# Optimization experiments

Hardware: AMD Instinct MI355X
Metric: run time of the kernel (lower is better)

The kernel has to match this reference:

```python
import jax, jax.numpy as jnp
import numpy as np

DIM = 1024
HEADS = 16
DIM_HEAD = 64
INNER = HEADS * DIM_HEAD
VID_LEN = 10
IMG_H, IMG_W = 16, 16
KS, KT = 5, 7  # kernel_spatial, kernel_temporal (causal=True)
BATCH = 1
SEQ = VID_LEN * IMG_H * IMG_W + 1  # +1 from causal pad -> 2561


def nearby_mask_causal(T, H, W, ks, kt):
    # numpy replication of generate_nearby_mask(causal=True); static, setup-time only
    te = (kt - 1) // 2
    frame = H * W
    S = T * frame
    p = ks // 2
    tmpl = (np.arange(ks * ks) >= (ks * ks) // 2).reshape(ks, ks)
    m = np.ones((S, T, H + 2 * p, W + 2 * p), dtype=bool)
    for t in range(T):
        for h in range(H):
            for w in range(W):
                i = t * frame + h * W + w
                m[i, t, h:h + ks, w:w + ks] = tmpl
                m[i, max(0, t - te):t, h:h + ks, w:w + ks] = False
    m = m[:, :, p:-p, p:-p].reshape(S, S)
    m = np.roll(m, -1, axis=0)
    m = np.pad(m, ((1, 0), (1, 0)), constant_values=True)
    m[0, 0] = False
    return m  # (S+1, S+1) bool; True = masked


def setup_inputs() -> dict:
    key = jax.random.key(0)
    ks = jax.random.split(key, 8)
    s = 0.02
    q = jax.random.normal(ks[0], (BATCH, SEQ, DIM), jnp.float32)
    k = jax.random.normal(ks[1], (BATCH, SEQ, DIM), jnp.float32)
    v = jax.random.normal(ks[2], (BATCH, SEQ, DIM), jnp.float32)
    Wq = jax.random.normal(ks[3], (DIM, INNER), jnp.float32) * s
    Wk = jax.random.normal(ks[4], (DIM, INNER), jnp.float32) * s
    Wv = jax.random.normal(ks[5], (DIM, INNER), jnp.float32) * s
    Wo = jax.random.normal(ks[6], (INNER, DIM), jnp.float32) * s
    bo = jnp.zeros((DIM,), jnp.float32)
    mask_block = jnp.asarray(nearby_mask_causal(VID_LEN, IMG_H, IMG_W, KS, KT))
    return {"q": q, "k": k, "v": v, "Wq": Wq, "Wk": Wk, "Wv": Wv,
            "Wo": Wo, "bo": bo, "mask_block": mask_block}


def reference(q, k, v, Wq, Wk, Wv, Wo, bo, mask_block):
    b, n, _ = q.shape
    h, dh = HEADS, DIM_HEAD
    scale = dh ** -0.5

    def heads_split(x, W):
        y = jnp.einsum('bnd,de->bne', x, W)
        return y.reshape(b, n, h, dh).transpose(0, 2, 1, 3)  # b h n dh

    qh = heads_split(q, Wq)
    kh = heads_split(k, Wk)
    vh = heads_split(v, Wv)
    dots = jnp.einsum('bhid,bhjd->bhij', qh, kh) * scale  # b h n n
    neg = -jnp.finfo(dots.dtype).max
    dots = jnp.where(mask_block[None, None], neg, dots)
    attn = jax.nn.softmax(dots, axis=-1)
    out = jnp.einsum('bhij,bhjd->bhid', attn, vh)
    out = out.transpose(0, 2, 1, 3).reshape(b, n, h * dh)
    out = jnp.einsum('bne,ed->bnd', out, Wo) + bo
    return out  # out[:, :n] is the identity here
```

## Files before the change

### kernel.cpp

```cpp
#include <hip/hip_runtime.h>
#include <float.h>

#define N_SEQ 2561
#define NPAD  2688
#define SEG   ((size_t)NPAD * 1024)
#define LOG2E 1.44269504088896340736f

typedef __attribute__((ext_vector_type(8))) short  short8;
typedef __attribute__((ext_vector_type(4))) short  s16x4;
typedef __attribute__((ext_vector_type(4))) float  f32x4;
typedef __attribute__((ext_vector_type(4))) unsigned int u32x4;
typedef __attribute__((ext_vector_type(4))) unsigned short u16x4;

__device__ __forceinline__ unsigned short f2bf(float f) {
  unsigned int u = __float_as_uint(f);
  u += 0x7FFFu + ((u >> 16) & 1u);
  return (unsigned short)(u >> 16);
}
__device__ __forceinline__ float bf2f(unsigned short v) {
  return __uint_as_float(((unsigned int)v) << 16);
}
__device__ __forceinline__ f32x4 mfma16(short8 a, short8 b, f32x4 c) {
  return __builtin_amdgcn_mfma_f32_16x16x32_bf16(a, b, c, 0, 0, 0);
}
__device__ __forceinline__ void load_lds16(const void* g, void* l) {
  __builtin_amdgcn_global_load_lds((const __attribute__((address_space(1))) void*)g,
                                   (__attribute__((address_space(3))) void*)l, 16, 0, 0);
}
__device__ __forceinline__ unsigned int cvt_pk_bf16(float a, float b) {
  unsigned int r;
  asm("v_cvt_pk_bf16_f32 %0, %1, %2" : "=v"(r) : "v"(a), "v"(b));
  return r;
}
__device__ __forceinline__ float fast_exp2(float x) {
  return __builtin_amdgcn_exp2f(x);
}

__global__ __launch_bounds__(256) void cvt_all(const float* __restrict__ q, const float* __restrict__ k,
                                               const float* __restrict__ v,
                                               const float* __restrict__ W0, const float* __restrict__ W1,
                                               const float* __restrict__ W2, const float* __restrict__ W3,
                                               unsigned short* __restrict__ Xq, unsigned short* __restrict__ Xk,
                                               unsigned short* __restrict__ Xv,
                                               unsigned short* __restrict__ T0, unsigned short* __restrict__ T1,
                                               unsigned short* __restrict__ T2, unsigned short* __restrict__ T3,
                                               uint2* __restrict__ Mtab) {
  __shared__ float tls[64][65];
  const int bid = blockIdx.x;
  if (bid < 4032) {
    const int by = bid / 1344, bx = bid - by * 1344;
    const float* src = (by == 0) ? q : (by == 1) ? k : v;
    unsigned short* dst = (by == 0) ? Xq : (by == 1) ? Xk : Xv;
    int idx = bx * 256 + threadIdx.x;
    size_t base = (size_t)idx * 8;
    int row = idx >> 7;
    short8 o;
    if (row < N_SEQ) {
      float4 a = *(const float4*)&src[base];
      float4 b = *(const float4*)&src[base + 4];
      o[0] = (short)f2bf(a.x); o[1] = (short)f2bf(a.y);
      o[2] = (short)f2bf(a.z); o[3] = (short)f2bf(a.w);
      o[4] = (short)f2bf(b.x); o[5] = (short)f2bf(b.y);
      o[6] = (short)f2bf(b.z); o[7] = (short)f2bf(b.w);
    } else {
      for (int j = 0; j < 8; ++j) o[j] = 0;
    }
    *(short8*)&dst[base] = o;
  } else if (bid < 5056) {
    const int b2 = bid - 4032;
    const int z = b2 >> 8, rem = b2 & 255;
    const int r0 = (rem >> 4) * 64, c0 = (rem & 15) * 64;
    const float* W; unsigned short* T; float scale = 1.0f;
    switch (z) {
      case 0: W = W0; T = T0; scale = 0.125f * LOG2E; break;
      case 1: W = W1; T = T1; break;
      case 2: W = W2; T = T2; break;
      default: W = W3; T = T3; break;
    }
    const int tid = threadIdx.x, tr = tid >> 4, tc = tid & 15;
#pragma unroll
    for (int u = 0; u < 4; ++u) {
      int row = tr + u * 16;
      float4 vv = *(const float4*)&W[(size_t)(r0 + row) * 1024 + c0 + tc * 4];
      tls[tc * 4 + 0][row] = vv.x; tls[tc * 4 + 1][row] = vv.y;
      tls[tc * 4 + 2][row] = vv.z; tls[tc * 4 + 3][row] = vv.w;
    }
    __syncthreads();
#pragma unroll
    for (int u = 0; u < 4; ++u) {
      int crow = tr + u * 16;
      u16x4 o;
#pragma unroll
      for (int j = 0; j < 4; ++j) o[j] = f2bf(tls[crow][tc * 4 + j] * scale);
      *(u16x4*)&T[(size_t)(c0 + crow) * 1024 + r0 + tc * 4] = o;
    }
  } else {
    const int idx = (bid - 5056) * 256 + threadIdx.x;
    const int r = idx >> 6, lane = idx & 63;
    const int lhi = lane >> 4, llo = lane & 15;
    const int rlo5 = min(max(r - 2, 0), 11);
    unsigned mpast = 0, mcur = 0;
#pragma unroll
    for (int n = 0; n < 6; ++n)
#pragma unroll
      for (int rr = 0; rr < 4; ++rr) {
        int s = n * 16 + lhi * 4 + rr;
        int u = rlo5 * 16 + s - 1;
        if (u < 0 || u > 255) continue;
        int rk = u >> 4, ck = u & 15;
        int dr = rk - r, dc = ck - llo;
        if (dr < -2 || dr > 2 || dc < -2 || dc > 2) continue;
        mpast |= 1u << (n * 4 + rr);
        if (dr < 0 || (dr == 0 && dc < 0)) mcur |= 1u << (n * 4 + rr);
      }
    Mtab[idx] = make_uint2(mpast, mcur);
  }
}

__device__ __forceinline__ void stage_tile(const unsigned short* A, const unsigned short* Bt,
                                           unsigned short* Asm, unsigned short* Bsm,
                                           int i0, int c0, int k0, int w, int srow, int scol) {
#pragma unroll
  for (int u = 0; u < 4; ++u) {
    int row = w * 32 + u * 8 + srow;
    load_lds16(&A [(size_t)(i0 + row) * 1024 + k0 + scol], &Asm[(w * 32 + u * 8) * 64]);
    load_lds16(&Bt[(size_t)(c0 + row) * 1024 + k0 + scol], &Bsm[(w * 32 + u * 8) * 64]);
  }
}

template <int MODE>
__device__ __forceinline__ void gemm_core(const unsigned short* A, const unsigned short* Bt,
                                          unsigned short* C, int i0, int c0,
                                          unsigned short* Asm, unsigned short* Bsm) {
  const int tid = threadIdx.x, w = tid >> 6, lane = tid & 63;
  const int wr = w >> 1, wc = w & 1;
  const int srow = lane >> 3;
  const int scol = ((lane & 7) * 8) ^ (srow << 3);
  f32x4 acc[4][4] = {};

  stage_tile(A, Bt, Asm, Bsm, i0, c0, 0, w, srow, scol);

  for (int t = 0; t < 16; ++t) {
    __syncthreads();
    if (t < 15)
      stage_tile(A, Bt, Asm + ((t + 1) & 1) * 8192, Bsm + ((t + 1) & 1) * 8192,
                 i0, c0, (t + 1) * 64, w, srow, scol);
    const unsigned short* Ab = Asm + (t & 1) * 8192;
    const unsigned short* Bb = Bsm + (t & 1) * 8192;
#pragma unroll
    for (int kk = 0; kk < 2; ++kk) {
      const int colel = kk * 32 + (lane >> 4) * 8;
      short8 af[4], bf[4];
#pragma unroll
      for (int m = 0; m < 4; ++m) {
        int row = wr * 64 + m * 16 + (lane & 15);
        af[m] = *(const short8*)&Ab[row * 64 + (colel ^ ((row & 7) << 3))];
      }
#pragma unroll
      for (int n = 0; n < 4; ++n) {
        int row = wc * 64 + n * 16 + (lane & 15);
        bf[n] = *(const short8*)&Bb[row * 64 + (colel ^ ((row & 7) << 3))];
      }
#pragma unroll
      for (int m = 0; m < 4; ++m)
#pragma unroll
        for (int n = 0; n < 4; ++n)
          acc[m][n] = mfma16(af[m], bf[n], acc[m][n]);
    }
  }

#pragma unroll
  for (int m = 0; m < 4; ++m)
#pragma unroll
    for (int n = 0; n < 4; ++n) {
      const int col = c0 + wc * 64 + n * 16 + (lane & 15);
#pragma unroll
      for (int r = 0; r < 4; ++r) {
        const int row = i0 + wr * 64 + m * 16 + (lane >> 4) * 4 + r;
        if (MODE == 1) {
          C[((size_t)(col >> 6) * NPAD + row) * 64 + (col & 63)] = f2bf(acc[m][n][r]);
        } else {
          C[(((size_t)(row >> 6) * 168 + (col >> 4)) * 64 + (row & 63)) * 16 + (col & 15)] = f2bf(acc[m][n][r]);
        }
      }
    }
}

__global__ __launch_bounds__(256) void proj3(const unsigned short* __restrict__ Xq, const unsigned short* __restrict__ WqT, unsigned short* __restrict__ Qh,
                                             const unsigned short* __restrict__ Xk, const unsigned short* __restrict__ WkT, unsigned short* __restrict__ Kh,
                                             const unsigned short* __restrict__ WvT, const unsigned short* __restrict__ Xv, unsigned short* __restrict__ Vt) {
  __shared__ unsigned short Asm[2 * 8192];
  __shared__ unsigned short Bsm[2 * 8192];
  int b = blockIdx.x;
  b = (b & 7) * 63 + (b >> 3);
  if (b < 168) {
    int r = b;
    gemm_core<1>(Xq, WqT, Qh, (r >> 3) * 128, (r & 7) * 128, Asm, Bsm);
  } else if (b < 336) {
    int r = b - 168;
    gemm_core<1>(Xk, WkT, Kh, (r >> 3) * 128, (r & 7) * 128, Asm, Bsm);
  } else {
    int r = b - 336;
    gemm_core<2>(WvT, Xv, Vt, (r / 21) * 128, (r % 21) * 128, Asm, Bsm);
  }
}

__global__ __launch_bounds__(256) void outproj(const unsigned short* __restrict__ A, const unsigned short* __restrict__ Bt,
                                               float* __restrict__ out, const float* __restrict__ bias) {
  __shared__ unsigned short Asm[2 * 4096];
  __shared__ unsigned short Bsm[2 * 8192];
  int b = (blockIdx.x & 7) * 42 + (blockIdx.x >> 3);
  const int i0 = (b >> 3) * 64, c0 = (b & 7) * 128;
  const int tid = threadIdx.x, w = tid >> 6, lane = tid & 63;
  const int wr = w >> 1, wc = w & 1;
  const int srow = lane >> 3;
  const int scol = ((lane & 7) * 8) ^ (srow << 3);
  const int llo = lane & 15, lhi = lane >> 4;
  f32x4 acc[2][4] = {};

#define STAGE64(buf, k0)                                                                     \
  {                                                                                          \
    _Pragma("unroll")                                                                        \
    for (int u = 0; u < 2; ++u) {                                                            \
      int row = w * 16 + u * 8 + srow;                                                       \
      load_lds16(&A[(size_t)(i0 + row) * 1024 + (k0) + scol], &Asm[(buf) * 4096 + (w * 16 + u * 8) * 64]); \
    }                                                                                        \
    _Pragma("unroll")                                                                        \
    for (int u = 0; u < 4; ++u) {                                                            \
      int row = w * 32 + u * 8 + srow;                                                       \
      load_lds16(&Bt[(size_t)(c0 + row) * 1024 + (k0) + scol], &Bsm[(buf) * 8192 + (w * 32 + u * 8) * 64]); \
    }                                                                                        \
  }

  STAGE64(0, 0)
  for (int t = 0; t < 16; ++t) {
    __syncthreads();
    if (t < 15) STAGE64((t + 1) & 1, (t + 1) * 64)
    const unsigned short* Ab = Asm + (t & 1) * 4096;
    const unsigned short* Bb = Bsm + (t & 1) * 8192;
#pragma unroll
    for (int kk = 0; kk < 2; ++kk) {
      const int colel = kk * 32 + lhi * 8;
      short8 af[2], bf[4];
#pragma unroll
      for (int m = 0; m < 2; ++m) {
        int row = wr * 32 + m * 16 + llo;
        af[m] = *(const short8*)&Ab[row * 64 + (colel ^ ((row & 7) << 3))];
      }
#pragma unroll
      for (int n = 0; n < 4; ++n) {
        int row = wc * 64 + n * 16 + llo;
        bf[n] = *(const short8*)&Bb[row * 64 + (colel ^ ((row & 7) << 3))];
      }
#pragma unroll
      for (int m = 0; m < 2; ++m)
#pragma unroll
        for (int n = 0; n < 4; ++n)
          acc[m][n] = mfma16(af[m], bf[n], acc[m][n]);
    }
  }
#undef STAGE64

#pragma unroll
  for (int m = 0; m < 2; ++m)
#pragma unroll
    for (int n = 0; n < 4; ++n) {
      const int col = c0 + wc * 64 + n * 16 + llo;
      const float bb = bias[col];
#pragma unroll
      for (int r = 0; r < 4; ++r) {
        const int row = i0 + wr * 32 + m * 16 + lhi * 4 + r;
        if (row < N_SEQ) out[(size_t)row * 1024 + col] = acc[m][n][r] + bb;
      }
    }
}

__global__ __launch_bounds__(256, 3) void attn_span4(const unsigned short* __restrict__ Qh,
                                                     const unsigned short* __restrict__ Kh,
                                                     const unsigned short* __restrict__ Vt,
                                                     unsigned short* __restrict__ Ob,
                                                     const uint2* __restrict__ Mtab) {
  __shared__ float Lacc[3][64][17];
  __shared__ float Ll[4][16];
  int bid = blockIdx.x + blockIdx.y * 160;
  bid = (bid & 7) * 320 + (bid >> 3);
  const int qg = bid % 160, h = bid / 160;
  const int w = threadIdx.x >> 6, lane = threadIdx.x & 63;
  const int lhi = lane >> 4, llo = lane & 15;
  const int t = qg >> 4, r = qg & 15;
  const int rlo5 = min(max(r - 2, 0), 11);
  const int f = t - 3 + w;

  const uint2 mm = Mtab[(r << 6) + lane];
  const unsigned msk = (w == 3) ? mm.y : mm.x;

  const unsigned short* qp = &Qh[((size_t)h * NPAD + qg * 16 + llo) * 64 + lhi * 8];
  short8 qf0 = *(const short8*)&qp[0];
  short8 qf1 = *(const short8*)&qp[32];

  short8 kf[6][2];
  s16x4  vv[3][4][2];
  if (f >= 0) {
    const int jb0 = f * 256 + rlo5 * 16;
    const unsigned short* kbase = &Kh[((size_t)h * NPAD + jb0) * 64];
#pragma unroll
    for (int n = 0; n < 6; ++n) {
      const unsigned short* kp = kbase + (n * 16 + llo) * 64;
      kf[n][0] = *(const short8*)&kp[lhi * 8];
      kf[n][1] = *(const short8*)&kp[32 + lhi * 8];
    }
    const size_t tb = (size_t)h * 168 + (jb0 >> 4);
#pragma unroll
    for (int kk = 0; kk < 3; ++kk)
#pragma unroll
      for (int n2 = 0; n2 < 4; ++n2) {
        vv[kk][n2][0] = *(const s16x4*)&Vt[((tb + kk * 2)     * 64 + n2 * 16 + llo) * 16 + lhi * 4];
        vv[kk][n2][1] = *(const s16x4*)&Vt[((tb + kk * 2 + 1) * 64 + n2 * 16 + llo) * 16 + lhi * 4];
      }
  }
  __builtin_amdgcn_sched_barrier(0);

  f32x4 acc[4] = {};
  float l = 0.f;

  if (f >= 0) {
    float p[6][4];
#pragma unroll
    for (int n = 0; n < 6; ++n) {
      f32x4 z = {0.f, 0.f, 0.f, 0.f};
      z = mfma16(kf[n][0], qf0, z);
      z = mfma16(kf[n][1], qf1, z);
#pragma unroll
      for (int rr = 0; rr < 4; ++rr) {
        float pv = ((msk >> (n * 4 + rr)) & 1u) ? fast_exp2(z[rr]) : 0.f;
        p[n][rr] = pv;
        l += pv;
      }
    }

#pragma unroll
    for (int kk = 0; kk < 3; ++kk) {
      const int n0 = kk * 2;
      u32x4 pw;
      pw[0] = cvt_pk_bf16(p[n0][0], p[n0][1]);
      pw[1] = cvt_pk_bf16(p[n0][2], p[n0][3]);
      pw[2] = cvt_pk_bf16(p[n0 + 1][0], p[n0 + 1][1]);
      pw[3] = cvt_pk_bf16(p[n0 + 1][2], p[n0 + 1][3]);
      short8 pf = __builtin_bit_cast(short8, pw);
#pragma unroll
      for (int n2 = 0; n2 < 4; ++n2) {
        short8 vf = __builtin_shufflevector(vv[kk][n2][0], vv[kk][n2][1], 0, 1, 2, 3, 4, 5, 6, 7);
        acc[n2] = mfma16(pf, vf, acc[n2]);
      }
    }
  }

  l += __shfl_xor(l, 16);
  l += __shfl_xor(l, 32);
  if (lhi == 0) Ll[w][llo] = l;
  if (w > 0) {
#pragma unroll
    for (int n2 = 0; n2 < 4; ++n2)
#pragma unroll
      for (int rr = 0; rr < 4; ++rr)
        Lacc[w - 1][lane][n2 * 4 + rr] = acc[n2][rr];
  }
  __syncthreads();
  if (w == 0) {
    const float lt = Ll[0][llo] + Ll[1][llo] + Ll[2][llo] + Ll[3][llo];
    float li[4];
#pragma unroll
    for (int rr = 0; rr < 4; ++rr) li[rr] = 1.0f / __shfl(lt, lhi * 4 + rr);
#pragma unroll
    for (int rr = 0; rr < 4; ++rr) {
      const int row = qg * 16 + lhi * 4 + rr;
#pragma unroll
      for (int n2 = 0; n2 < 4; ++n2) {
        float s = acc[n2][rr] + Lacc[0][lane][n2 * 4 + rr]
                              + Lacc[1][lane][n2 * 4 + rr]
                              + Lacc[2][lane][n2 * 4 + rr];
        Ob[(size_t)row * 1024 + h * 64 + n2 * 16 + llo] = f2bf(s * li[rr]);
      }
    }
  }
}

__global__ void fix_rows(const unsigned short* __restrict__ Vt, unsigned short* __restrict__ Ob) {
  const int d = blockIdx.x, lane = threadIdx.x;
  const int h = d >> 6, dd = d & 63;
  const int kb4 = lane >> 4, ks = lane & 15;
  float s = 0.f;
  for (int kb = kb4; kb < 168; kb += 4)
    s += bf2f(Vt[(((size_t)h * 168 + kb) * 64 + dd) * 16 + ks]);
  s += __shfl_xor(s, 1);  s += __shfl_xor(s, 2);  s += __shfl_xor(s, 4);
  s += __shfl_xor(s, 8);  s += __shfl_xor(s, 16); s += __shfl_xor(s, 32);
  if (lane == 0) {
    Ob[(size_t)2560 * 1024 + d] = f2bf(s * (1.0f / 2561.0f));
    Ob[d] = Vt[((size_t)h * 168 * 64 + dd) * 16];
  }
}

extern "C" void kernel_launch(void* const* d_in, const int* in_sizes, int n_in,
                              void* d_out, int out_size, void* d_ws, size_t ws_size,
                              hipStream_t stream) {
  const float* q  = (const float*)d_in[0];
  const float* k  = (const float*)d_in[1];
  const float* v  = (const float*)d_in[2];
  const float* Wq = (const float*)d_in[3];
  const float* Wk = (const float*)d_in[4];
  const float* Wv = (const float*)d_in[5];
  const float* Wo = (const float*)d_in[6];
  const float* bo = (const float*)d_in[7];

  unsigned short* ws = (unsigned short*)d_ws;
  const size_t MW = (size_t)1024 * 1024;
  unsigned short* Xq  = ws;
  unsigned short* Xk  = ws + SEG;
  unsigned short* Xv  = ws + 2 * SEG;
  unsigned short* Qh  = ws + 3 * SEG;
  unsigned short* Kh  = ws + 4 * SEG;
  unsigned short* Vt  = ws + 5 * SEG;
  unsigned short* WqT = ws + 6 * SEG;
  unsigned short* WkT = WqT + MW;
  unsigned short* WvT = WqT + 2 * MW;
  unsigned short* WoT = WqT + 3 * MW;
  uint2* Mtab = (uint2*)(WqT + 4 * MW);
  unsigned short* ObB = Xq;

  cvt_all<<<5060, 256, 0, stream>>>(q, k, v, Wq, Wk, Wv, Wo, Xq, Xk, Xv, WqT, WkT, WvT, WoT, Mtab);

  proj3<<<504, 256, 0, stream>>>(Xq, WqT, Qh, Xk, WkT, Kh, WvT, Xv, Vt);

  attn_span4<<<dim3(160, 16), 256, 0, stream>>>(Qh, Kh, Vt, ObB, Mtab);
  fix_rows<<<1024, 64, 0, stream>>>(Vt, ObB);

  outproj<<<336, 256, 0, stream>>>(ObB, WoT, (float*)d_out, bo);
}
```

Baseline: 96.36 us.

## Duplicate V tiles into overlapping layout, fold fix_rows into attention kernel

The V projection epilogue now writes each 16-key group twice, into a 32-wide overlapping layout, so the attention kernel can load each V fragment with one 16-byte short8 load instead of two 8-byte loads plus a shuffle. The separate fix_rows kernel is folded into attn_span5 as an extra column of blocks, which removes one launch. s_setprio is raised around the MFMA section. In exchange the V workspace doubles in size, the proj3 epilogue does extra scattered stores, and the weight buffers are moved to make room.

Result: slower. 204.5 us (+112.3%).

```diff
diff --git a/kernel.cpp b/kernel.cpp
--- a/kernel.cpp
+++ b/kernel.cpp
@@ -180,7 +180,13 @@
         if (MODE == 1) {
           C[((size_t)(col >> 6) * NPAD + row) * 64 + (col & 63)] = f2bf(acc[m][n][r]);
         } else {
-          C[(((size_t)(row >> 6) * 168 + (col >> 4)) * 64 + (row & 63)) * 16 + (col & 15)] = f2bf(acc[m][n][r]);
+          const int h = row >> 6, dd = row & 63;
+          const int g = col >> 4;
+          const int kp = ((col >> 2) & 3) * 8 + (col & 3);
+          const unsigned short val = f2bf(acc[m][n][r]);
+          C[(((size_t)h * 168 + g) * 64 + dd) * 32 + kp] = val;
+          if (g > 0)
+            C[(((size_t)h * 168 + g - 1) * 64 + dd) * 32 + kp + 4] = val;
         }
       }
     }
@@ -275,13 +281,33 @@
     }
 }
 
-__global__ __launch_bounds__(256, 3) void attn_span4(const unsigned short* __restrict__ Qh,
+__global__ __launch_bounds__(256, 3) void attn_span5(const unsigned short* __restrict__ Qh,
                                                      const unsigned short* __restrict__ Kh,
                                                      const unsigned short* __restrict__ Vt,
                                                      unsigned short* __restrict__ Ob,
                                                      const uint2* __restrict__ Mtab) {
   __shared__ float Lacc[3][64][17];
   __shared__ float Ll[4][16];
+
+  if (blockIdx.x == 160) {
+    const int h = blockIdx.y;
+    const int tid = threadIdx.x;
+    const int dd = tid >> 2, sub = tid & 3;
+    float s = 0.f;
+    for (int i = sub; i < 2688; i += 4) {
+      int g = i >> 4, k16 = i & 15;
+      int kp = ((k16 >> 2) << 3) + (k16 & 3);
+      s += bf2f(Vt[(((size_t)h * 168 + g) * 64 + dd) * 32 + kp]);
+    }
+    s += __shfl_xor(s, 1);
+    s += __shfl_xor(s, 2);
+    if (sub == 0) {
+      Ob[(size_t)2560 * 1024 + h * 64 + dd] = f2bf(s * (1.0f / 2561.0f));
+      Ob[h * 64 + dd] = Vt[(((size_t)h * 168) * 64 + dd) * 32];
+    }
+    return;
+  }
+
   int bid = blockIdx.x + blockIdx.y * 160;
   bid = (bid & 7) * 320 + (bid >> 3);
   const int qg = bid % 160, h = bid / 160;
@@ -299,7 +325,7 @@
   short8 qf1 = *(const short8*)&qp[32];
 
   short8 kf[6][2];
-  s16x4  vv[3][4][2];
+  short8 vf[3][4];
   if (f >= 0) {
     const int jb0 = f * 256 + rlo5 * 16;
     const unsigned short* kbase = &Kh[((size_t)h * NPAD + jb0) * 64];
@@ -313,10 +339,8 @@
 #pragma unroll
     for (int kk = 0; kk < 3; ++kk)
 #pragma unroll
-      for (int n2 = 0; n2 < 4; ++n2) {
-        vv[kk][n2][0] = *(const s16x4*)&Vt[((tb + kk * 2)     * 64 + n2 * 16 + llo) * 16 + lhi * 4];
-        vv[kk][n2][1] = *(const s16x4*)&Vt[((tb + kk * 2 + 1) * 64 + n2 * 16 + llo) * 16 + lhi * 4];
-      }
+      for (int n2 = 0; n2 < 4; ++n2)
+        vf[kk][n2] = *(const short8*)&Vt[((tb + kk * 2) * 64 + n2 * 16 + llo) * 32 + lhi * 8];
   }
   __builtin_amdgcn_sched_barrier(0);
 
@@ -324,6 +348,7 @@
   float l = 0.f;
 
   if (f >= 0) {
+    __builtin_amdgcn_s_setprio(1);
     float p[6][4];
 #pragma unroll
     for (int n = 0; n < 6; ++n) {
@@ -348,11 +373,10 @@
       pw[3] = cvt_pk_bf16(p[n0 + 1][2], p[n0 + 1][3]);
       short8 pf = __builtin_bit_cast(short8, pw);
 #pragma unroll
-      for (int n2 = 0; n2 < 4; ++n2) {
-        short8 vf = __builtin_shufflevector(vv[kk][n2][0], vv[kk][n2][1], 0, 1, 2, 3, 4, 5, 6, 7);
-        acc[n2] = mfma16(pf, vf, acc[n2]);
-      }
-    }
+      for (int n2 = 0; n2 < 4; ++n2)
+        acc[n2] = mfma16(pf, vf[kk][n2], acc[n2]);
+    }
+    __builtin_amdgcn_s_setprio(0);
   }
 
   l += __shfl_xor(l, 16);
@@ -382,21 +406,6 @@
         Ob[(size_t)row * 1024 + h * 64 + n2 * 16 + llo] = f2bf(s * li[rr]);
       }
     }
-  }
-}
-
-__global__ void fix_rows(const unsigned short* __restrict__ Vt, unsigned short* __restrict__ Ob) {
-  const int d = blockIdx.x, lane = threadIdx.x;
-  const int h = d >> 6, dd = d & 63;
-  const int kb4 = lane >> 4, ks = lane & 15;
-  float s = 0.f;
-  for (int kb = kb4; kb < 168; kb += 4)
-    s += bf2f(Vt[(((size_t)h * 168 + kb) * 64 + dd) * 16 + ks]);
-  s += __shfl_xor(s, 1);  s += __shfl_xor(s, 2);  s += __shfl_xor(s, 4);
-  s += __shfl_xor(s, 8);  s += __shfl_xor(s, 16); s += __shfl_xor(s, 32);
-  if (lane == 0) {
-    Ob[(size_t)2560 * 1024 + d] = f2bf(s * (1.0f / 2561.0f));
-    Ob[d] = Vt[((size_t)h * 168 * 64 + dd) * 16];
   }
 }
 
@@ -420,7 +429,7 @@
   unsigned short* Qh  = ws + 3 * SEG;
   unsigned short* Kh  = ws + 4 * SEG;
   unsigned short* Vt  = ws + 5 * SEG;
-  unsigned short* WqT = ws + 6 * SEG;
+  unsigned short* WqT = ws + 7 * SEG;
   unsigned short* WkT = WqT + MW;
   unsigned short* WvT = WqT + 2 * MW;
   unsigned short* WoT = WqT + 3 * MW;
@@ -431,8 +440,7 @@
 
   proj3<<<504, 256, 0, stream>>>(Xq, WqT, Qh, Xk, WkT, Kh, WvT, Xv, Vt);
 
-  attn_span4<<<dim3(160, 16), 256, 0, stream>>>(Qh, Kh, Vt, ObB, Mtab);
-  fix_rows<<<1024, 64, 0, stream>>>(Vt, ObB);
+  attn_span5<<<dim3(161, 16), 256, 0, stream>>>(Qh, Kh, Vt, ObB, Mtab);
 
   outproj<<<336, 256, 0, stream>>>(ObB, WoT, (float*)d_out, bo);
 }
```
